# Optimization experiments

Measured on AMD Instinct MI355X. Metric: run time of the kernel, lower is better.

The kernel has to match this reference:

```python
import jax, jax.numpy as jnp
import numpy as np

B = 8192            # batch.size
NNZ = B * 32        # active features per position ~32
FT = 512            # ft_out
F_FULL = 49152      # HalfKA feature count
F_VIRT = 768        # factorized (virtual) feature count


def setup_inputs() -> dict:
    key = jax.random.key(0)
    ks = jax.random.split(key, 8)
    s_ft = 1.0 / np.sqrt(F_FULL).astype(np.float32)
    s_fft = 1.0 / np.sqrt(F_VIRT).astype(np.float32)
    s_out = 1.0 / np.sqrt(2 * FT).astype(np.float32)
    return {
        "values": jnp.ones((NNZ,), dtype=jnp.float32),
        # W_ft stored feature-major [F_FULL, FT] = torch ft.weight.T, so rows are gathered per feature
        "W_ft": jax.random.uniform(ks[0], (F_FULL, FT), jnp.float32, -s_ft, s_ft),
        "ft_b": jax.random.uniform(ks[1], (FT,), jnp.float32, -s_ft, s_ft),
        "W_fft": jax.random.uniform(ks[2], (F_VIRT, FT), jnp.float32, -s_fft, s_fft),
        "fft_b": jax.random.uniform(ks[3], (FT,), jnp.float32, -s_fft, s_fft),
        "W_out": jax.random.uniform(ks[4], (1, 2 * FT), jnp.float32, -s_out, s_out),
        "out_b": jax.random.uniform(ks[5], (1,), jnp.float32, -s_out, s_out),
        "batch_ids": jnp.sort(jax.random.randint(ks[6], (NNZ,), 0, B)),
        "stm_feat": jax.random.randint(ks[7], (NNZ,), 0, F_FULL),
        "nstm_feat": jax.random.randint(jax.random.fold_in(key, 7), (NNZ,), 0, F_FULL),
        "size": B,
    }


def reference(values, W_ft, ft_b, W_fft, fft_b, W_out, out_b,
              batch_ids, stm_feat, nstm_feat, size):
    v = values[:, None]  # [NNZ, 1]

    def transform(feat):
        # sparse COO x dense weight == gather weight rows per active feature, scale, segment-sum
        acc = jax.ops.segment_sum(W_ft[feat] * v, batch_ids, num_segments=size)
        acc_v = jax.ops.segment_sum(W_fft[feat % F_VIRT] * v, batch_ids, num_segments=size)
        return acc + acc_v + ft_b + fft_b  # both Linear biases applied once per row

    stm_ft = transform(stm_feat)    # [B, FT]
    nstm_ft = transform(nstm_feat)  # [B, FT]
    hidden = jnp.clip(jnp.concatenate([stm_ft, nstm_ft], axis=1), 0.0, 1.0)
    return jax.nn.sigmoid(hidden @ W_out.T + out_b)  # [B, 1]
```

## Files before the change

### kernel.cpp

```cpp
#include <hip/hip_runtime.h>
#include <hip/hip_bf16.h>
#include <math.h>


constexpr int FT      = 512;
constexpr int FV      = 768;
constexpr int THREADS = 128;
constexpr int CHUNK   = 128;

typedef __attribute__((ext_vector_type(8))) unsigned short ushort8_t;

__device__ inline unsigned short f2bf(float x) {
    union { float f; unsigned int u; } v; v.f = x;
    unsigned int r = v.u + 0x7FFFu + ((v.u >> 16) & 1u);
    return (unsigned short)(r >> 16);
}
__device__ inline float bf2f(unsigned short s) {
    union { unsigned int u; float f; } v; v.u = ((unsigned int)s) << 16;
    return v.f;
}

__global__ __launch_bounds__(256)
void convert_kernel(const float* __restrict__ W_ft, const float* __restrict__ W_fft,
                    unsigned short* __restrict__ ft_bf, unsigned short* __restrict__ fft_bf,
                    int n8_ft, int n8_total)
{
    int i = blockIdx.x * 256 + threadIdx.x;
    if (i >= n8_total) return;
    const float* src; unsigned short* dst; int base;
    if (i < n8_ft) { src = W_ft;  dst = ft_bf;  base = i * 8; }
    else           { src = W_fft; dst = fft_bf; base = (i - n8_ft) * 8; }
    const float4 f0 = *(const float4*)(src + base);
    const float4 f1 = *(const float4*)(src + base + 4);
    ushort8_t u;
    u[0] = f2bf(f0.x); u[1] = f2bf(f0.y); u[2] = f2bf(f0.z); u[3] = f2bf(f0.w);
    u[4] = f2bf(f1.x); u[5] = f2bf(f1.y); u[6] = f2bf(f1.z); u[7] = f2bf(f1.w);
    *(ushort8_t*)(dst + base) = u;
}

__global__ __launch_bounds__(THREADS)
void nnue_bf16_kernel(const float* __restrict__ values,
                      const unsigned short* __restrict__ Wft,
                      const float* __restrict__ ft_b,
                      const unsigned short* __restrict__ Wfft,
                      const float* __restrict__ fft_b,
                      const float* __restrict__ W_out,
                      const float* __restrict__ out_b,
                      const int*   __restrict__ batch_ids,
                      const int*   __restrict__ stm_feat,
                      const int*   __restrict__ nstm_feat,
                      int nnz,
                      float* __restrict__ out)
{
    const int b    = blockIdx.x;
    const int t    = threadIdx.x;
    const int w    = t >> 6;
    const int lane = t & 63;
    const int col  = lane * 8;

    int lo0 = 0, hi0 = nnz;
    while (lo0 < hi0) {
        int mid = (lo0 + hi0) >> 1;
        if (batch_ids[mid] < b) lo0 = mid + 1; else hi0 = mid;
    }
    int lo1 = lo0, hi1 = nnz;
    while (lo1 < hi1) {
        int mid = (lo1 + hi1) >> 1;
        if (batch_ids[mid] < b + 1) lo1 = mid + 1; else hi1 = mid;
    }
    const int seg_lo = lo0, seg_hi = lo1;

    __shared__ int   sh_off_s [CHUNK];
    __shared__ int   sh_off_sv[CHUNK];
    __shared__ int   sh_off_n [CHUNK];
    __shared__ int   sh_off_nv[CHUNK];
    __shared__ float sh_v     [CHUNK];
    __shared__ float sh_comb  [2][FT];

    float acc_s[8] = {0,0,0,0,0,0,0,0};
    float acc_n[8] = {0,0,0,0,0,0,0,0};

    for (int base = seg_lo; base < seg_hi; base += CHUNK) {
        const int cnt = min(CHUNK, seg_hi - base);
        __syncthreads();
        if (t < cnt) {
            int fs = stm_feat[base + t];
            int fn = nstm_feat[base + t];
            sh_off_s [t] = fs * FT;
            sh_off_sv[t] = (fs % FV) * FT;
            sh_off_n [t] = fn * FT;
            sh_off_nv[t] = (fn % FV) * FT;
            sh_v     [t] = values[base + t];
        }
        __syncthreads();

        #pragma unroll 4
        for (int j = w; j < cnt; j += 2) {
            const float v = sh_v[j];
            const ushort8_t a  = *(const ushort8_t*)(Wft  + sh_off_s [j] + col);
            const ushort8_t av = *(const ushort8_t*)(Wfft + sh_off_sv[j] + col);
            const ushort8_t c  = *(const ushort8_t*)(Wft  + sh_off_n [j] + col);
            const ushort8_t cv = *(const ushort8_t*)(Wfft + sh_off_nv[j] + col);
            #pragma unroll
            for (int k = 0; k < 8; ++k) {
                acc_s[k] = fmaf(bf2f(a[k]) + bf2f(av[k]), v, acc_s[k]);
                acc_n[k] = fmaf(bf2f(c[k]) + bf2f(cv[k]), v, acc_n[k]);
            }
        }
    }

    __syncthreads();
    if (w == 1) {
        #pragma unroll
        for (int k = 0; k < 8; ++k) {
            sh_comb[0][col + k] = acc_s[k];
            sh_comb[1][col + k] = acc_n[k];
        }
    }
    __syncthreads();

    if (w == 0) {
        #pragma unroll
        for (int k = 0; k < 8; ++k) {
            acc_s[k] += sh_comb[0][col + k];
            acc_n[k] += sh_comb[1][col + k];
        }

        const float4 fb0 = *(const float4*)(ft_b  + col);
        const float4 fb1 = *(const float4*)(ft_b  + col + 4);
        const float4 vb0 = *(const float4*)(fft_b + col);
        const float4 vb1 = *(const float4*)(fft_b + col + 4);
        const float4 ws0 = *(const float4*)(W_out + col);
        const float4 ws1 = *(const float4*)(W_out + col + 4);
        const float4 wn0 = *(const float4*)(W_out + FT + col);
        const float4 wn1 = *(const float4*)(W_out + FT + col + 4);

        const float bias[8] = { fb0.x + vb0.x, fb0.y + vb0.y, fb0.z + vb0.z, fb0.w + vb0.w,
                                fb1.x + vb1.x, fb1.y + vb1.y, fb1.z + vb1.z, fb1.w + vb1.w };
        const float wos[8]  = { ws0.x, ws0.y, ws0.z, ws0.w, ws1.x, ws1.y, ws1.z, ws1.w };
        const float won[8]  = { wn0.x, wn0.y, wn0.z, wn0.w, wn1.x, wn1.y, wn1.z, wn1.w };

        float partial = 0.f;
        #pragma unroll
        for (int k = 0; k < 8; ++k) {
            float hs = fminf(fmaxf(acc_s[k] + bias[k], 0.f), 1.f);
            float hn = fminf(fmaxf(acc_n[k] + bias[k], 0.f), 1.f);
            partial = fmaf(hs, wos[k], partial);
            partial = fmaf(hn, won[k], partial);
        }

        #pragma unroll
        for (int off = 32; off > 0; off >>= 1)
            partial += __shfl_down(partial, off, 64);

        if (lane == 0)
            out[b] = 1.0f / (1.0f + expf(-(partial + out_b[0])));
    }
}

__global__ __launch_bounds__(THREADS)
void nnue_f32_kernel(const float* __restrict__ values,
                     const float* __restrict__ W_ft,
                     const float* __restrict__ ft_b,
                     const float* __restrict__ W_fft,
                     const float* __restrict__ fft_b,
                     const float* __restrict__ W_out,
                     const float* __restrict__ out_b,
                     const int*   __restrict__ batch_ids,
                     const int*   __restrict__ stm_feat,
                     const int*   __restrict__ nstm_feat,
                     int nnz,
                     float* __restrict__ out)
{
    const int b   = blockIdx.x;
    const int t   = threadIdx.x;
    const int col = t * 4;

    int lo0 = 0, hi0 = nnz;
    while (lo0 < hi0) {
        int mid = (lo0 + hi0) >> 1;
        if (batch_ids[mid] < b) lo0 = mid + 1; else hi0 = mid;
    }
    int lo1 = lo0, hi1 = nnz;
    while (lo1 < hi1) {
        int mid = (lo1 + hi1) >> 1;
        if (batch_ids[mid] < b + 1) lo1 = mid + 1; else hi1 = mid;
    }
    const int seg_lo = lo0, seg_hi = lo1;

    __shared__ int   sh_off_s [CHUNK];
    __shared__ int   sh_off_sv[CHUNK];
    __shared__ int   sh_off_n [CHUNK];
    __shared__ int   sh_off_nv[CHUNK];
    __shared__ float sh_v     [CHUNK];

    float4 acc_s = make_float4(0.f, 0.f, 0.f, 0.f);
    float4 acc_n = make_float4(0.f, 0.f, 0.f, 0.f);

    for (int base = seg_lo; base < seg_hi; base += CHUNK) {
        const int cnt = min(CHUNK, seg_hi - base);
        __syncthreads();
        if (t < cnt) {
            int fs = stm_feat[base + t];
            int fn = nstm_feat[base + t];
            sh_off_s [t] = fs * FT;
            sh_off_sv[t] = (fs % FV) * FT;
            sh_off_n [t] = fn * FT;
            sh_off_nv[t] = (fn % FV) * FT;
            sh_v     [t] = values[base + t];
        }
        __syncthreads();

        #pragma unroll 2
        for (int j = 0; j < cnt; ++j) {
            const float v = sh_v[j];
            const float4 a  = *(const float4*)(W_ft  + sh_off_s [j] + col);
            const float4 av = *(const float4*)(W_fft + sh_off_sv[j] + col);
            const float4 c  = *(const float4*)(W_ft  + sh_off_n [j] + col);
            const float4 cv = *(const float4*)(W_fft + sh_off_nv[j] + col);
            acc_s.x = fmaf(a.x + av.x, v, acc_s.x);
            acc_s.y = fmaf(a.y + av.y, v, acc_s.y);
            acc_s.z = fmaf(a.z + av.z, v, acc_s.z);
            acc_s.w = fmaf(a.w + av.w, v, acc_s.w);
            acc_n.x = fmaf(c.x + cv.x, v, acc_n.x);
            acc_n.y = fmaf(c.y + cv.y, v, acc_n.y);
            acc_n.z = fmaf(c.z + cv.z, v, acc_n.z);
            acc_n.w = fmaf(c.w + cv.w, v, acc_n.w);
        }
    }

    const float4 fb  = *(const float4*)(ft_b  + col);
    const float4 vb  = *(const float4*)(fft_b + col);
    const float4 wos = *(const float4*)(W_out + col);
    const float4 won = *(const float4*)(W_out + FT + col);

    float partial = 0.f;
    {
        float h;
        h = fminf(fmaxf(acc_s.x + fb.x + vb.x, 0.f), 1.f); partial = fmaf(h, wos.x, partial);
        h = fminf(fmaxf(acc_s.y + fb.y + vb.y, 0.f), 1.f); partial = fmaf(h, wos.y, partial);
        h = fminf(fmaxf(acc_s.z + fb.z + vb.z, 0.f), 1.f); partial = fmaf(h, wos.z, partial);
        h = fminf(fmaxf(acc_s.w + fb.w + vb.w, 0.f), 1.f); partial = fmaf(h, wos.w, partial);
        h = fminf(fmaxf(acc_n.x + fb.x + vb.x, 0.f), 1.f); partial = fmaf(h, won.x, partial);
        h = fminf(fmaxf(acc_n.y + fb.y + vb.y, 0.f), 1.f); partial = fmaf(h, won.y, partial);
        h = fminf(fmaxf(acc_n.z + fb.z + vb.z, 0.f), 1.f); partial = fmaf(h, won.z, partial);
        h = fminf(fmaxf(acc_n.w + fb.w + vb.w, 0.f), 1.f); partial = fmaf(h, won.w, partial);
    }

    #pragma unroll
    for (int off = 32; off > 0; off >>= 1)
        partial += __shfl_down(partial, off, 64);

    __shared__ float wave_sum[THREADS / 64];
    if ((t & 63) == 0) wave_sum[t >> 6] = partial;
    __syncthreads();
    if (t == 0) {
        float s = wave_sum[0] + wave_sum[1] + out_b[0];
        out[b] = 1.0f / (1.0f + expf(-s));
    }
}

extern "C" void kernel_launch(void* const* d_in, const int* in_sizes, int n_in,
                              void* d_out, int out_size, void* d_ws, size_t ws_size,
                              hipStream_t stream) {
    const float* values    = (const float*)d_in[0];
    const float* W_ft      = (const float*)d_in[1];
    const float* ft_b      = (const float*)d_in[2];
    const float* W_fft     = (const float*)d_in[3];
    const float* fft_b     = (const float*)d_in[4];
    const float* W_out     = (const float*)d_in[5];
    const float* out_b     = (const float*)d_in[6];
    const int*   batch_ids = (const int*)d_in[7];
    const int*   stm_feat  = (const int*)d_in[8];
    const int*   nstm_feat = (const int*)d_in[9];

    const int nnz    = in_sizes[0];
    const int B      = out_size;
    const int n_ft   = in_sizes[1];
    const int n_fft  = in_sizes[3];

    const size_t need = (size_t)(n_ft + n_fft) * sizeof(unsigned short);

    if (ws_size >= need) {
        unsigned short* ft_bf  = (unsigned short*)d_ws;
        unsigned short* fft_bf = ft_bf + n_ft;
        const int n8_ft    = n_ft / 8;
        const int n8_total = (n_ft + n_fft) / 8;
        const int cgrid    = (n8_total + 255) / 256;
        convert_kernel<<<cgrid, 256, 0, stream>>>(W_ft, W_fft, ft_bf, fft_bf,
                                                  n8_ft, n8_total);
        nnue_bf16_kernel<<<B, THREADS, 0, stream>>>(
            values, ft_bf, ft_b, fft_bf, fft_b, W_out, out_b,
            batch_ids, stm_feat, nstm_feat, nnz, (float*)d_out);
    } else {
        nnue_f32_kernel<<<B, THREADS, 0, stream>>>(
            values, W_ft, ft_b, W_fft, fft_b, W_out, out_b,
            batch_ids, stm_feat, nstm_feat, nnz, (float*)d_out);
    }
}
```

Baseline: 236.7 us.

## Pre-fold factorized weights into combined bf16 table to halve gathers

The conversion kernel now adds W_fft[f % 768] into each W_ft row before rounding to bf16, so it writes a single combined table. The main kernel gathers one row per active feature per perspective instead of two, which halves gather traffic and drops the modulo work. The trade-off is a slightly heavier conversion pass, since every W_ft row also reads a W_fft row. Rounding the sum once rather than each term separately changes numerics a little.

```diff
diff --git a/kernel.cpp b/kernel.cpp
--- a/kernel.cpp
+++ b/kernel.cpp
@@ -22,27 +22,32 @@
 
 __global__ __launch_bounds__(256)
 void convert_kernel(const float* __restrict__ W_ft, const float* __restrict__ W_fft,
-                    unsigned short* __restrict__ ft_bf, unsigned short* __restrict__ fft_bf,
-                    int n8_ft, int n8_total)
+                    unsigned short* __restrict__ comb, int n8)
 {
     int i = blockIdx.x * 256 + threadIdx.x;
-    if (i >= n8_total) return;
-    const float* src; unsigned short* dst; int base;
-    if (i < n8_ft) { src = W_ft;  dst = ft_bf;  base = i * 8; }
-    else           { src = W_fft; dst = fft_bf; base = (i - n8_ft) * 8; }
-    const float4 f0 = *(const float4*)(src + base);
-    const float4 f1 = *(const float4*)(src + base + 4);
+    if (i >= n8) return;
+    const int f    = i >> 6;
+    const int gcol = (i & 63) * 8;
+    const int base = i * 8;
+    const int vrow = (f % FV) * FT + gcol;
+
+    const float4 a0 = *(const float4*)(W_ft  + base);
+    const float4 a1 = *(const float4*)(W_ft  + base + 4);
+    const float4 b0 = *(const float4*)(W_fft + vrow);
+    const float4 b1 = *(const float4*)(W_fft + vrow + 4);
+
     ushort8_t u;
-    u[0] = f2bf(f0.x); u[1] = f2bf(f0.y); u[2] = f2bf(f0.z); u[3] = f2bf(f0.w);
-    u[4] = f2bf(f1.x); u[5] = f2bf(f1.y); u[6] = f2bf(f1.z); u[7] = f2bf(f1.w);
-    *(ushort8_t*)(dst + base) = u;
+    u[0] = f2bf(a0.x + b0.x); u[1] = f2bf(a0.y + b0.y);
+    u[2] = f2bf(a0.z + b0.z); u[3] = f2bf(a0.w + b0.w);
+    u[4] = f2bf(a1.x + b1.x); u[5] = f2bf(a1.y + b1.y);
+    u[6] = f2bf(a1.z + b1.z); u[7] = f2bf(a1.w + b1.w);
+    *(ushort8_t*)(comb + base) = u;
 }
 
 __global__ __launch_bounds__(THREADS)
-void nnue_bf16_kernel(const float* __restrict__ values,
-                      const unsigned short* __restrict__ Wft,
+void nnue_comb_kernel(const float* __restrict__ values,
+                      const unsigned short* __restrict__ Wc,
                       const float* __restrict__ ft_b,
-                      const unsigned short* __restrict__ Wfft,
                       const float* __restrict__ fft_b,
                       const float* __restrict__ W_out,
                       const float* __restrict__ out_b,
@@ -70,12 +75,10 @@
     }
     const int seg_lo = lo0, seg_hi = lo1;
 
-    __shared__ int   sh_off_s [CHUNK];
-    __shared__ int   sh_off_sv[CHUNK];
-    __shared__ int   sh_off_n [CHUNK];
-    __shared__ int   sh_off_nv[CHUNK];
-    __shared__ float sh_v     [CHUNK];
-    __shared__ float sh_comb  [2][FT];
+    __shared__ int   sh_off_s[CHUNK];
+    __shared__ int   sh_off_n[CHUNK];
+    __shared__ float sh_v    [CHUNK];
+    __shared__ float sh_comb [2][FT];
 
     float acc_s[8] = {0,0,0,0,0,0,0,0};
     float acc_n[8] = {0,0,0,0,0,0,0,0};
@@ -84,27 +87,21 @@
         const int cnt = min(CHUNK, seg_hi - base);
         __syncthreads();
         if (t < cnt) {
-            int fs = stm_feat[base + t];
-            int fn = nstm_feat[base + t];
-            sh_off_s [t] = fs * FT;
-            sh_off_sv[t] = (fs % FV) * FT;
-            sh_off_n [t] = fn * FT;
-            sh_off_nv[t] = (fn % FV) * FT;
-            sh_v     [t] = values[base + t];
+            sh_off_s[t] = stm_feat [base + t] * FT;
+            sh_off_n[t] = nstm_feat[base + t] * FT;
+            sh_v    [t] = values[base + t];
         }
         __syncthreads();
 
         #pragma unroll 4
         for (int j = w; j < cnt; j += 2) {
             const float v = sh_v[j];
-            const ushort8_t a  = *(const ushort8_t*)(Wft  + sh_off_s [j] + col);
-            const ushort8_t av = *(const ushort8_t*)(Wfft + sh_off_sv[j] + col);
-            const ushort8_t c  = *(const ushort8_t*)(Wft  + sh_off_n [j] + col);
-            const ushort8_t cv = *(const ushort8_t*)(Wfft + sh_off_nv[j] + col);
+            const ushort8_t a = *(const ushort8_t*)(Wc + sh_off_s[j] + col);
+            const ushort8_t c = *(const ushort8_t*)(Wc + sh_off_n[j] + col);
             #pragma unroll
             for (int k = 0; k < 8; ++k) {
-                acc_s[k] = fmaf(bf2f(a[k]) + bf2f(av[k]), v, acc_s[k]);
-                acc_n[k] = fmaf(bf2f(c[k]) + bf2f(cv[k]), v, acc_n[k]);
+                acc_s[k] = fmaf(bf2f(a[k]), v, acc_s[k]);
+                acc_n[k] = fmaf(bf2f(c[k]), v, acc_n[k]);
             }
         }
     }
@@ -274,23 +271,19 @@
     const int*   stm_feat  = (const int*)d_in[8];
     const int*   nstm_feat = (const int*)d_in[9];
 
-    const int nnz    = in_sizes[0];
-    const int B      = out_size;
-    const int n_ft   = in_sizes[1];
-    const int n_fft  = in_sizes[3];
-
-    const size_t need = (size_t)(n_ft + n_fft) * sizeof(unsigned short);
+    const int nnz  = in_sizes[0];
+    const int B    = out_size;
+    const int n_ft = in_sizes[1];
+
+    const size_t need = (size_t)n_ft * sizeof(unsigned short);
 
     if (ws_size >= need) {
-        unsigned short* ft_bf  = (unsigned short*)d_ws;
-        unsigned short* fft_bf = ft_bf + n_ft;
-        const int n8_ft    = n_ft / 8;
-        const int n8_total = (n_ft + n_fft) / 8;
-        const int cgrid    = (n8_total + 255) / 256;
-        convert_kernel<<<cgrid, 256, 0, stream>>>(W_ft, W_fft, ft_bf, fft_bf,
-                                                  n8_ft, n8_total);
-        nnue_bf16_kernel<<<B, THREADS, 0, stream>>>(
-            values, ft_bf, ft_b, fft_bf, fft_b, W_out, out_b,
+        unsigned short* comb = (unsigned short*)d_ws;
+        const int n8    = n_ft / 8;
+        const int cgrid = (n8 + 255) / 256;
+        convert_kernel<<<cgrid, 256, 0, stream>>>(W_ft, W_fft, comb, n8);
+        nnue_comb_kernel<<<B, THREADS, 0, stream>>>(
+            values, comb, ft_b, fft_b, W_out, out_b,
             batch_ids, stm_feat, nstm_feat, nnz, (float*)d_out);
     } else {
         nnue_f32_kernel<<<B, THREADS, 0, stream>>>(
```

Result: faster. 230.2 us (-2.8%).
